# Performance work log

Measured on AMD Instinct MI355X. Metric: run time of the kernel, lower is better.

Reference implementation:

```python
import jax, jax.numpy as jnp
import numpy as np

N, IN_F, OUT_F, G = 8192, 1024, 1024, 5


def setup_inputs() -> dict:
    key = jax.random.key(0)
    k1, k2 = jax.random.split(key)
    x = jax.random.normal(k1, (N, IN_F), dtype=jnp.float32)
    spline_weights = jax.random.normal(k2, (OUT_F, IN_F, G), dtype=jnp.float32) * 0.1
    return {"x": x, "spline_weights": spline_weights}


def reference(x, spline_weights):
    out_f, in_f, g = spline_weights.shape
    grid = jnp.linspace(-1.0, 1.0, g).astype(x.dtype)
    leading = x.shape[:-1]
    xf = x.reshape(-1, in_f)                       # [N, in]
    x_c = jnp.clip(jnp.tanh(xf), grid[0], grid[-1])
    # bucket index: number of grid points <= x_c, minus 1, clamped to [0, g-2]
    idx = jnp.sum(x_c[..., None] >= grid, axis=-1) - 1
    idx = jnp.clip(idx, 0, g - 2)                  # [N, in] int
    idx_r = jnp.minimum(idx + 1, g - 1)
    g_left = grid[idx]
    g_right = grid[idx_r]
    t = (x_c - g_left) / (g_right - g_left + 1e-8)  # [N, in]
    # sparse interpolation coefficients over the grid axis: two nonzeros per (n,i)
    oh_l = jax.nn.one_hot(idx, g, dtype=xf.dtype)   # [N, in, G]
    oh_r = jax.nn.one_hot(idx_r, g, dtype=xf.dtype)
    coeff = (1.0 - t)[..., None] * oh_l + t[..., None] * oh_r  # [N, in, G]
    # y[n,o] = sum_i (1-t) * W[o,i,idx] + t * W[o,i,idx+1]
    out = jnp.einsum('nig,oig->no', coeff, spline_weights)
    return out.reshape(*leading, out_f)
```

## Files before the change

### kernel.cpp

```cpp
#include <hip/hip_runtime.h>
#include <stdint.h>

#define N_ROWS 8192
#define IN_F   1024
#define OUT_F  1024
#define NG     5
#define KTOT   (IN_F * NG)

#define BM 128
#define BN 128
#define BK 64
#define NKT (KTOT / BK)

typedef float          f32x4 __attribute__((ext_vector_type(4)));
typedef short          s16x8 __attribute__((ext_vector_type(8)));
typedef unsigned short u16x8 __attribute__((ext_vector_type(8)));

__device__ __forceinline__ unsigned short f2bf_rne(float f) {
    unsigned u = __float_as_uint(f);
    u = (u + 0x7fffu + ((u >> 16) & 1u)) >> 16;
    return (unsigned short)u;
}
__device__ __forceinline__ float bf2f(unsigned short h) {
    return __uint_as_float(((unsigned)h) << 16);
}

__device__ __forceinline__ void gload_lds16(const void* g, void* l) {
    __builtin_amdgcn_global_load_lds(
        (const __attribute__((address_space(1))) unsigned int*)g,
        (__attribute__((address_space(3))) unsigned int*)l, 16, 0, 0);
}

__global__ __launch_bounds__(256) void prep_p(const float* __restrict__ x,
                                              unsigned short* __restrict__ P) {
    int t = blockIdx.x * 256 + threadIdx.x;
    float4 v = reinterpret_cast<const float4*>(x)[t];
    float r[4] = {v.x, v.y, v.z, v.w};
    ushort4 o;
    unsigned short* po = (unsigned short*)&o;
#pragma unroll
    for (int j = 0; j < 4; ++j) {
        float xc = fminf(fmaxf(r[j], -9.0f), 9.0f);
        float e  = __expf(2.0f * xc);
        float th = (e - 1.0f) / (e + 1.0f);
        po[j] = (unsigned short)__float2uint_rn((th + 1.0f) * 32767.0f);
    }
    reinterpret_cast<ushort4*>(P)[t] = o;
}

__global__ __launch_bounds__(256) void prep_w(const float* __restrict__ W,
                                              unsigned short* __restrict__ Wh,
                                              unsigned short* __restrict__ Wl) {
    int t = blockIdx.x * 256 + threadIdx.x;
    int o = t >> 10, i = t & 1023;
    const float* wp = W + (size_t)o * KTOT + i * NG;
#pragma unroll
    for (int g = 0; g < NG; ++g) {
        float w = wp[g];
        unsigned short h = f2bf_rne(w);
        unsigned short l = f2bf_rne(w - bf2f(h));
        int dst = o * KTOT + g * 1024 + i;
        Wh[dst] = h;
        Wl[dst] = l;
    }
}

struct SLds {
    unsigned short Ah[BM * BK];
    unsigned short Al[BM * BK];
    unsigned short Bh[BN * BK];
    unsigned short Bl[BN * BK];
};

__global__ __launch_bounds__(256, 2) void kan_gemm(
        const unsigned short* __restrict__ P,
        const unsigned short* __restrict__ Wh,
        const unsigned short* __restrict__ Wl,
        float* __restrict__ out) {
    __shared__ SLds s;

    int bid = blockIdx.x;
    int wg  = (bid & 7) * 64 + (bid >> 3);
    int nb  = wg >> 6;
    int mb  = wg & 63;
    int n0 = mb * BM, o0 = nb * BN;

    int tid  = threadIdx.x;
    int lane = tid & 63, wid = tid >> 6;
    int wm = wid >> 1, wn = wid & 1;

    int aoff[4], adst[4];
#pragma unroll
    for (int r = 0; r < 4; ++r) {
        int f = tid + r * 256, row = f >> 3, ks = f & 7;
        aoff[r] = (n0 + row) * IN_F + ks * 8;
        adst[r] = row * BK + ((ks ^ (row & 7)) << 3);
    }
    int bks = (lane & 7) ^ (lane >> 3);
    int boff[4];
#pragma unroll
    for (int q = 0; q < 4; ++q)
        boff[q] = (o0 + wid * 32 + q * 8 + (lane >> 3)) * KTOT + bks * 8;
    int arow_f = wm * 64 + (lane & 15);
    int brow_f = wn * 64 + (lane & 15);
    int sl0    = lane >> 4;

    f32x4 acc[4][4] = {};

    u16x8 ucur[4], unext[4];
#pragma unroll
    for (int r = 0; r < 4; ++r)
        ucur[r] = *reinterpret_cast<const u16x8*>(&P[aoff[r]]);

    for (int kt = 0; kt < NKT; ++kt) {
        int k0 = kt * BK;
        int g  = k0 >> 10;
        float gv = -1.0f + 0.5f * (float)g;
        int i0n = ((kt + 1 < NKT) ? (kt + 1) * BK : 0) & 1023;

        __syncthreads();

#pragma unroll
        for (int q = 0; q < 4; ++q) {
            int ldsrow = (wid * 32 + q * 8) * BK;
            gload_lds16(Wh + boff[q] + k0, &s.Bh[ldsrow]);
            gload_lds16(Wl + boff[q] + k0, &s.Bl[ldsrow]);
        }
#pragma unroll
        for (int r = 0; r < 4; ++r)
            unext[r] = *reinterpret_cast<const u16x8*>(&P[aoff[r] + i0n]);

#pragma unroll
        for (int r = 0; r < 4; ++r) {
            u16x8 hv, lv;
#pragma unroll
            for (int j = 0; j < 8; ++j) {
                float xc = fmaf((float)ucur[r][j], (1.0f / 32767.0f), -1.0f);
                float c  = fmaxf(0.0f, fmaf(-2.0f, fabsf(xc - gv), 1.0f));
                unsigned hb = __float_as_uint(c) >> 16;
                hv[j] = (unsigned short)hb;
                float hi = __uint_as_float(hb << 16);
                lv[j] = (unsigned short)(__float_as_uint(c - hi) >> 16);
            }
            *reinterpret_cast<u16x8*>(&s.Ah[adst[r]]) = hv;
            *reinterpret_cast<u16x8*>(&s.Al[adst[r]]) = lv;
        }
#pragma unroll
        for (int r = 0; r < 4; ++r) ucur[r] = unext[r];

        __syncthreads();

#pragma unroll
        for (int kk = 0; kk < 2; ++kk) {
            s16x8 ah[4], al[4], bh[4], bl[4];
#pragma unroll
            for (int m = 0; m < 4; ++m) {
                int row  = arow_f + m * 16;
                int slot = (kk * 4 + sl0) ^ (row & 7);
                ah[m] = *reinterpret_cast<const s16x8*>(&s.Ah[row * BK + slot * 8]);
                al[m] = *reinterpret_cast<const s16x8*>(&s.Al[row * BK + slot * 8]);
            }
#pragma unroll
            for (int nf = 0; nf < 4; ++nf) {
                int row  = brow_f + nf * 16;
                int slot = (kk * 4 + sl0) ^ (row & 7);
                bh[nf] = *reinterpret_cast<const s16x8*>(&s.Bh[row * BK + slot * 8]);
                bl[nf] = *reinterpret_cast<const s16x8*>(&s.Bl[row * BK + slot * 8]);
            }
#pragma unroll
            for (int m = 0; m < 4; ++m)
#pragma unroll
                for (int nf = 0; nf < 4; ++nf) {
                    acc[m][nf] = __builtin_amdgcn_mfma_f32_16x16x32_bf16(
                                     ah[m], bh[nf], acc[m][nf], 0, 0, 0);
                    acc[m][nf] = __builtin_amdgcn_mfma_f32_16x16x32_bf16(
                                     ah[m], bl[nf], acc[m][nf], 0, 0, 0);
                    acc[m][nf] = __builtin_amdgcn_mfma_f32_16x16x32_bf16(
                                     al[m], bh[nf], acc[m][nf], 0, 0, 0);
                }
        }
    }

    int rb = n0 + wm * 64 + (lane >> 4) * 4;
    int cb = o0 + wn * 64 + (lane & 15);
#pragma unroll
    for (int m = 0; m < 4; ++m)
#pragma unroll
        for (int nf = 0; nf < 4; ++nf)
#pragma unroll
            for (int jj = 0; jj < 4; ++jj)
                out[(size_t)(rb + m * 16 + jj) * OUT_F + cb + nf * 16] =
                    acc[m][nf][jj];
}

__global__ __launch_bounds__(256) void kan_naive(const float* __restrict__ x,
                                                 const float* __restrict__ W,
                                                 float* __restrict__ out) {
    int bn = blockIdx.x & 3;
    int bm = blockIdx.x >> 2;
    int o = bn * 256 + threadIdx.x;
    int nbase = bm * 16;
    float acc[16];
#pragma unroll
    for (int j = 0; j < 16; ++j) acc[j] = 0.0f;
    for (int i = 0; i < IN_F; ++i) {
        const float* wp = &W[(size_t)o * KTOT + i * NG];
        float w0 = wp[0], w1 = wp[1], w2 = wp[2], w3 = wp[3], w4 = wp[4];
#pragma unroll
        for (int j = 0; j < 16; ++j) {
            float xc = tanhf(x[(size_t)(nbase + j) * IN_F + i]);
            float c0 = fmaxf(0.f, fmaf(-2.f, fabsf(xc + 1.0f), 1.f));
            float c1 = fmaxf(0.f, fmaf(-2.f, fabsf(xc + 0.5f), 1.f));
            float c2 = fmaxf(0.f, fmaf(-2.f, fabsf(xc), 1.f));
            float c3 = fmaxf(0.f, fmaf(-2.f, fabsf(xc - 0.5f), 1.f));
            float c4 = fmaxf(0.f, fmaf(-2.f, fabsf(xc - 1.0f), 1.f));
            acc[j] += c0 * w0 + c1 * w1 + c2 * w2 + c3 * w3 + c4 * w4;
        }
    }
#pragma unroll
    for (int j = 0; j < 16; ++j)
        out[(size_t)(nbase + j) * OUT_F + o] = acc[j];
}

extern "C" void kernel_launch(void* const* d_in, const int* in_sizes, int n_in,
                              void* d_out, int out_size, void* d_ws, size_t ws_size,
                              hipStream_t stream) {
    const float* x = (const float*)d_in[0];
    const float* W = (const float*)d_in[1];
    float* out = (float*)d_out;

    const size_t P_BYTES = (size_t)N_ROWS * IN_F * 2;
    const size_t WPLANE  = (size_t)OUT_F * KTOT * 2;

    if (ws_size >= P_BYTES + 2 * WPLANE) {
        unsigned short* P  = (unsigned short*)d_ws;
        unsigned short* Wh = (unsigned short*)((char*)d_ws + P_BYTES);
        unsigned short* Wl = (unsigned short*)((char*)d_ws + P_BYTES + WPLANE);
        prep_p<<<(N_ROWS * IN_F / 4) / 256, 256, 0, stream>>>(x, P);
        prep_w<<<(OUT_F * IN_F) / 256, 256, 0, stream>>>(W, Wh, Wl);
        kan_gemm<<<512, 256, 0, stream>>>(P, Wh, Wl, out);
    } else {
        kan_naive<<<2048, 256, 0, stream>>>(x, W, out);
    }
}
```

Measured before the change: 307.7 us.

## Precompute A hi/lo planes and double-buffer a pure async-LDS GEMM

When the workspace is large enough, a new prep kernel expands tanh(x) into full bf16 hi/lo coefficient planes over all grid points. A pure GEMM then streams both A and B into LDS with direct global-to-LDS loads, double-buffered with BK=32 and one barrier per step. This removes per-tile coefficient computation and the register staging of A from the main loop. The cost is a larger workspace and more HBM traffic, since the A planes are about 5x wider than the quantized P. A mid fallback kernel with a different tile shape and a vectorized prep_w are also added.

```diff
diff --git a/kernel.cpp b/kernel.cpp
--- a/kernel.cpp
+++ b/kernel.cpp
@@ -7,11 +7,6 @@
 #define NG     5
 #define KTOT   (IN_F * NG)
 
-#define BM 128
-#define BN 128
-#define BK 64
-#define NKT (KTOT / BK)
-
 typedef float          f32x4 __attribute__((ext_vector_type(4)));
 typedef short          s16x8 __attribute__((ext_vector_type(8)));
 typedef unsigned short u16x8 __attribute__((ext_vector_type(8)));
@@ -24,60 +19,88 @@
 __device__ __forceinline__ float bf2f(unsigned short h) {
     return __uint_as_float(((unsigned)h) << 16);
 }
-
 __device__ __forceinline__ void gload_lds16(const void* g, void* l) {
     __builtin_amdgcn_global_load_lds(
         (const __attribute__((address_space(1))) unsigned int*)g,
         (__attribute__((address_space(3))) unsigned int*)l, 16, 0, 0);
 }
 
-__global__ __launch_bounds__(256) void prep_p(const float* __restrict__ x,
-                                              unsigned short* __restrict__ P) {
+__global__ __launch_bounds__(256) void prep_a(const float* __restrict__ x,
+                                              unsigned short* __restrict__ Ahp,
+                                              unsigned short* __restrict__ Alp) {
     int t = blockIdx.x * 256 + threadIdx.x;
-    float4 v = reinterpret_cast<const float4*>(x)[t];
-    float r[4] = {v.x, v.y, v.z, v.w};
-    ushort4 o;
-    unsigned short* po = (unsigned short*)&o;
-#pragma unroll
-    for (int j = 0; j < 4; ++j) {
-        float xc = fminf(fmaxf(r[j], -9.0f), 9.0f);
-        float e  = __expf(2.0f * xc);
-        float th = (e - 1.0f) / (e + 1.0f);
-        po[j] = (unsigned short)__float2uint_rn((th + 1.0f) * 32767.0f);
-    }
-    reinterpret_cast<ushort4*>(P)[t] = o;
+    int n = t >> 7, i8 = t & 127;
+    const float4* xp = reinterpret_cast<const float4*>(x + (size_t)n * IN_F + i8 * 8);
+    float4 a = xp[0], b = xp[1];
+    float r[8] = {a.x, a.y, a.z, a.w, b.x, b.y, b.z, b.w};
+    float xc[8];
+#pragma unroll
+    for (int j = 0; j < 8; ++j) {
+        float v = fminf(fmaxf(r[j], -9.0f), 9.0f);
+        float e = __expf(2.0f * v);
+        xc[j] = (e - 1.0f) / (e + 1.0f);
+    }
+    size_t base = (size_t)n * KTOT + i8 * 8;
+#pragma unroll
+    for (int g = 0; g < NG; ++g) {
+        float gv = -1.0f + 0.5f * (float)g;
+        u16x8 hv, lv;
+#pragma unroll
+        for (int j = 0; j < 8; ++j) {
+            float c  = fmaxf(0.0f, fmaf(-2.0f, fabsf(xc[j] - gv), 1.0f));
+            unsigned hb = __float_as_uint(c) >> 16;
+            hv[j] = (unsigned short)hb;
+            lv[j] = (unsigned short)(__float_as_uint(c - __uint_as_float(hb << 16)) >> 16);
+        }
+        *reinterpret_cast<u16x8*>(&Ahp[base + g * 1024]) = hv;
+        *reinterpret_cast<u16x8*>(&Alp[base + g * 1024]) = lv;
+    }
 }
 
 __global__ __launch_bounds__(256) void prep_w(const float* __restrict__ W,
                                               unsigned short* __restrict__ Wh,
                                               unsigned short* __restrict__ Wl) {
-    int t = blockIdx.x * 256 + threadIdx.x;
-    int o = t >> 10, i = t & 1023;
-    const float* wp = W + (size_t)o * KTOT + i * NG;
+    int t  = blockIdx.x * 256 + threadIdx.x;
+    int o  = t >> 8, i4 = (t & 255) * 4;
+    const float4* wp = reinterpret_cast<const float4*>(W + (size_t)o * KTOT + i4 * NG);
+    float f[20];
+#pragma unroll
+    for (int q = 0; q < 5; ++q) {
+        float4 v = wp[q];
+        f[q*4+0] = v.x; f[q*4+1] = v.y; f[q*4+2] = v.z; f[q*4+3] = v.w;
+    }
 #pragma unroll
     for (int g = 0; g < NG; ++g) {
-        float w = wp[g];
-        unsigned short h = f2bf_rne(w);
-        unsigned short l = f2bf_rne(w - bf2f(h));
-        int dst = o * KTOT + g * 1024 + i;
-        Wh[dst] = h;
-        Wl[dst] = l;
-    }
-}
-
-struct SLds {
-    unsigned short Ah[BM * BK];
-    unsigned short Al[BM * BK];
-    unsigned short Bh[BN * BK];
-    unsigned short Bl[BN * BK];
-};
-
-__global__ __launch_bounds__(256, 2) void kan_gemm(
-        const unsigned short* __restrict__ P,
+        ushort4 hq, lq;
+        unsigned short* hp = (unsigned short*)&hq;
+        unsigned short* lp = (unsigned short*)&lq;
+#pragma unroll
+        for (int di = 0; di < 4; ++di) {
+            float w = f[di * NG + g];
+            unsigned short h = f2bf_rne(w);
+            hp[di] = h;
+            lp[di] = f2bf_rne(w - bf2f(h));
+        }
+        int dst = o * KTOT + g * 1024 + i4;
+        *reinterpret_cast<ushort4*>(&Wh[dst]) = hq;
+        *reinterpret_cast<ushort4*>(&Wl[dst]) = lq;
+    }
+}
+
+#define BM 128
+#define BN 128
+#define PBK 32
+#define PNKT (KTOT / PBK)
+
+struct SLdsDB { unsigned short d[2][4][BM * PBK]; };
+
+__global__ __launch_bounds__(256, 2) void kan_gemm_pure(
+        const unsigned short* __restrict__ Ahp,
+        const unsigned short* __restrict__ Alp,
         const unsigned short* __restrict__ Wh,
         const unsigned short* __restrict__ Wl,
         float* __restrict__ out) {
-    __shared__ SLds s;
+    __shared__ SLdsDB s;
 
     int bid = blockIdx.x;
     int wg  = (bid & 7) * 64 + (bid >> 3);
@@ -89,100 +112,192 @@
     int lane = tid & 63, wid = tid >> 6;
     int wm = wid >> 1, wn = wid & 1;
 
-    int aoff[4], adst[4];
-#pragma unroll
-    for (int r = 0; r < 4; ++r) {
-        int f = tid + r * 256, row = f >> 3, ks = f & 7;
-        aoff[r] = (n0 + row) * IN_F + ks * 8;
-        adst[r] = row * BK + ((ks ^ (row & 7)) << 3);
-    }
-    int bks = (lane & 7) ^ (lane >> 3);
-    int boff[4];
+    int ks = (lane & 3) ^ ((lane >> 3) & 3);
+    int gA[2], gB[2], ldsb[2];
+#pragma unroll
+    for (int q = 0; q < 2; ++q) {
+        int r = wid * 32 + q * 16 + (lane >> 2);
+        gA[q] = (n0 + r) * KTOT + ks * 8;
+        gB[q] = (o0 + r) * KTOT + ks * 8;
+        ldsb[q] = (wid * 32 + q * 16) * PBK;
+    }
+    int sl0  = lane >> 4;
+    int arow = wm * 64 + (lane & 15);
+    int brow = wn * 64 + (lane & 15);
+    int aaddr = arow * PBK + ((sl0 ^ ((arow >> 1) & 3)) << 3);
+    int baddr = brow * PBK + ((sl0 ^ ((brow >> 1) & 3)) << 3);
+
+    f32x4 acc[4][4] = {};
+
+    auto STAGE = [&](int buf, int k0) {
+#pragma unroll
+        for (int q = 0; q < 2; ++q) {
+            gload_lds16(Ahp + gA[q] + k0, &s.d[buf][0][ldsb[q]]);
+            gload_lds16(Alp + gA[q] + k0, &s.d[buf][1][ldsb[q]]);
+            gload_lds16(Wh  + gB[q] + k0, &s.d[buf][2][ldsb[q]]);
+            gload_lds16(Wl  + gB[q] + k0, &s.d[buf][3][ldsb[q]]);
+        }
+    };
+    auto COMPUTE = [&](int buf) {
+        s16x8 ah[4], al[4], bh[4], bl[4];
+#pragma unroll
+        for (int m = 0; m < 4; ++m) {
+            ah[m] = *reinterpret_cast<const s16x8*>(&s.d[buf][0][aaddr + m * 512]);
+            al[m] = *reinterpret_cast<const s16x8*>(&s.d[buf][1][aaddr + m * 512]);
+        }
+#pragma unroll
+        for (int nf = 0; nf < 4; ++nf) {
+            bh[nf] = *reinterpret_cast<const s16x8*>(&s.d[buf][2][baddr + nf * 512]);
+            bl[nf] = *reinterpret_cast<const s16x8*>(&s.d[buf][3][baddr + nf * 512]);
+        }
+#pragma unroll
+        for (int m = 0; m < 4; ++m)
+#pragma unroll
+            for (int nf = 0; nf < 4; ++nf) {
+                acc[m][nf] = __builtin_amdgcn_mfma_f32_16x16x32_bf16(
+                                 ah[m], bh[nf], acc[m][nf], 0, 0, 0);
+                acc[m][nf] = __builtin_amdgcn_mfma_f32_16x16x32_bf16(
+                                 ah[m], bl[nf], acc[m][nf], 0, 0, 0);
+                acc[m][nf] = __builtin_amdgcn_mfma_f32_16x16x32_bf16(
+                                 al[m], bh[nf], acc[m][nf], 0, 0, 0);
+            }
+    };
+
+    STAGE(0, 0);
+    __syncthreads();
+    int cur = 0;
+    for (int kt = 0; kt < PNKT - 1; ++kt) {
+        STAGE(cur ^ 1, (kt + 1) * PBK);
+        COMPUTE(cur);
+        __syncthreads();
+        cur ^= 1;
+    }
+    COMPUTE(cur);
+
+    int rb = n0 + wm * 64 + (lane >> 4) * 4;
+    int cb = o0 + wn * 64 + (lane & 15);
+#pragma unroll
+    for (int m = 0; m < 4; ++m)
+#pragma unroll
+        for (int nf = 0; nf < 4; ++nf)
+#pragma unroll
+            for (int jj = 0; jj < 4; ++jj)
+                out[(size_t)(rb + m * 16 + jj) * OUT_F + cb + nf * 16] =
+                    acc[m][nf][jj];
+}
+
+__global__ __launch_bounds__(256) void prep_p(const float* __restrict__ x,
+                                              unsigned short* __restrict__ P) {
+    int t = blockIdx.x * 256 + threadIdx.x;
+    float4 a = reinterpret_cast<const float4*>(x)[t * 2];
+    float4 b = reinterpret_cast<const float4*>(x)[t * 2 + 1];
+    float r[8] = {a.x, a.y, a.z, a.w, b.x, b.y, b.z, b.w};
+    u16x8 o;
+#pragma unroll
+    for (int j = 0; j < 8; ++j) {
+        float xc = fminf(fmaxf(r[j], -9.0f), 9.0f);
+        float e  = __expf(2.0f * xc);
+        float th = (e - 1.0f) / (e + 1.0f);
+        o[j] = (unsigned short)__float2uint_rn((th + 1.0f) * 32767.0f);
+    }
+    *reinterpret_cast<u16x8*>(&P[(size_t)t * 8]) = o;
+}
+
+#define MBM 64
+#define MBN 256
+#define MBK 32
+struct SLdsM {
+    unsigned short Ah[4 * MBM * 8];
+    unsigned short Al[4 * MBM * 8];
+    unsigned short Bh[4 * MBN * 8];
+    unsigned short Bl[4 * MBN * 8];
+};
+
+__global__ __launch_bounds__(256, 3) void kan_gemm_mid(
+        const unsigned short* __restrict__ P,
+        const unsigned short* __restrict__ Wh,
+        const unsigned short* __restrict__ Wl,
+        float* __restrict__ out) {
+    __shared__ SLdsM s;
+    int bid = blockIdx.x;
+    int wg  = (bid & 7) * 64 + (bid >> 3);
+    int nb  = wg >> 7, mb = wg & 127;
+    int n0 = mb * MBM, o0 = nb * MBN;
+    int tid  = threadIdx.x;
+    int lane = tid & 63, w = tid >> 6;
+
+    int arow = tid >> 2, aks = tid & 3;
+    int agoff = (n0 + arow) * IN_F + aks * 8;
+    int aldst = aks * (MBM * 8) + arow * 8;
+    int brow4 = tid >> 2, bchunk = tid & 3;
+    int bldst = bchunk * (MBN * 8) + brow4 * 8;
+    int bgq[4];
 #pragma unroll
     for (int q = 0; q < 4; ++q)
-        boff[q] = (o0 + wid * 32 + q * 8 + (lane >> 3)) * KTOT + bks * 8;
-    int arow_f = wm * 64 + (lane & 15);
-    int brow_f = wn * 64 + (lane & 15);
-    int sl0    = lane >> 4;
+        bgq[q] = (o0 + q * 64 + brow4) * KTOT + bchunk * 8;
+    int fchunk = lane >> 4, fr = lane & 15;
 
     f32x4 acc[4][4] = {};
-
-    u16x8 ucur[4], unext[4];
-#pragma unroll
-    for (int r = 0; r < 4; ++r)
-        ucur[r] = *reinterpret_cast<const u16x8*>(&P[aoff[r]]);
-
-    for (int kt = 0; kt < NKT; ++kt) {
-        int k0 = kt * BK;
-        int g  = k0 >> 10;
-        float gv = -1.0f + 0.5f * (float)g;
-        int i0n = ((kt + 1 < NKT) ? (kt + 1) * BK : 0) & 1023;
-
+    for (int kt = 0; kt < KTOT / MBK; ++kt) {
+        int k0 = kt * MBK;
+        float gv = -1.0f + 0.5f * (float)(kt >> 5);
+        int i0 = (kt & 31) * MBK;
         __syncthreads();
-
-#pragma unroll
-        for (int q = 0; q < 4; ++q) {
-            int ldsrow = (wid * 32 + q * 8) * BK;
-            gload_lds16(Wh + boff[q] + k0, &s.Bh[ldsrow]);
-            gload_lds16(Wl + boff[q] + k0, &s.Bl[ldsrow]);
-        }
-#pragma unroll
-        for (int r = 0; r < 4; ++r)
-            unext[r] = *reinterpret_cast<const u16x8*>(&P[aoff[r] + i0n]);
-
-#pragma unroll
-        for (int r = 0; r < 4; ++r) {
+        u16x8 bregh[4], bregl[4];
+#pragma unroll
+        for (int q = 0; q < 4; ++q)
+            bregh[q] = *reinterpret_cast<const u16x8*>(&Wh[bgq[q] + k0]);
+#pragma unroll
+        for (int q = 0; q < 4; ++q)
+            bregl[q] = *reinterpret_cast<const u16x8*>(&Wl[bgq[q] + k0]);
+        {
+            u16x8 u = *reinterpret_cast<const u16x8*>(&P[agoff + i0]);
             u16x8 hv, lv;
 #pragma unroll
             for (int j = 0; j < 8; ++j) {
-                float xc = fmaf((float)ucur[r][j], (1.0f / 32767.0f), -1.0f);
+                float xc = fmaf((float)u[j], (1.0f / 32767.0f), -1.0f);
                 float c  = fmaxf(0.0f, fmaf(-2.0f, fabsf(xc - gv), 1.0f));
                 unsigned hb = __float_as_uint(c) >> 16;
                 hv[j] = (unsigned short)hb;
-                float hi = __uint_as_float(hb << 16);
-                lv[j] = (unsigned short)(__float_as_uint(c - hi) >> 16);
+                lv[j] = (unsigned short)(__float_as_uint(c - __uint_as_float(hb << 16)) >> 16);
             }
-            *reinterpret_cast<u16x8*>(&s.Ah[adst[r]]) = hv;
-            *reinterpret_cast<u16x8*>(&s.Al[adst[r]]) = lv;
-        }
-#pragma unroll
-        for (int r = 0; r < 4; ++r) ucur[r] = unext[r];
-
+            *reinterpret_cast<u16x8*>(&s.Ah[aldst]) = hv;
+            *reinterpret_cast<u16x8*>(&s.Al[aldst]) = lv;
+        }
+#pragma unroll
+        for (int q = 0; q < 4; ++q) {
+            *reinterpret_cast<u16x8*>(&s.Bh[bldst + q * 512]) = bregh[q];
+            *reinterpret_cast<u16x8*>(&s.Bl[bldst + q * 512]) = bregl[q];
+        }
         __syncthreads();
 
-#pragma unroll
-        for (int kk = 0; kk < 2; ++kk) {
-            s16x8 ah[4], al[4], bh[4], bl[4];
-#pragma unroll
-            for (int m = 0; m < 4; ++m) {
-                int row  = arow_f + m * 16;
-                int slot = (kk * 4 + sl0) ^ (row & 7);
-                ah[m] = *reinterpret_cast<const s16x8*>(&s.Ah[row * BK + slot * 8]);
-                al[m] = *reinterpret_cast<const s16x8*>(&s.Al[row * BK + slot * 8]);
+        s16x8 ah[4], al[4], bh[4], bl[4];
+#pragma unroll
+        for (int m = 0; m < 4; ++m) {
+            int e = fchunk * (MBM * 8) + (m * 16 + fr) * 8;
+            ah[m] = *reinterpret_cast<const s16x8*>(&s.Ah[e]);
+            al[m] = *reinterpret_cast<const s16x8*>(&s.Al[e]);
+        }
+#pragma unroll
+        for (int nf = 0; nf < 4; ++nf) {
+            int e = fchunk * (MBN * 8) + (w * 64 + nf * 16 + fr) * 8;
+            bh[nf] = *reinterpret_cast<const s16x8*>(&s.Bh[e]);
+            bl[nf] = *reinterpret_cast<const s16x8*>(&s.Bl[e]);
+        }
+#pragma unroll
+        for (int m = 0; m < 4; ++m)
+#pragma unroll
+            for (int nf = 0; nf < 4; ++nf) {
+                acc[m][nf] = __builtin_amdgcn_mfma_f32_16x16x32_bf16(
+                                 ah[m], bh[nf], acc[m][nf], 0, 0, 0);
+                acc[m][nf] = __builtin_amdgcn_mfma_f32_16x16x32_bf16(
+                                 ah[m], bl[nf], acc[m][nf], 0, 0, 0);
+                acc[m][nf] = __builtin_amdgcn_mfma_f32_16x16x32_bf16(
+                                 al[m], bh[nf], acc[m][nf], 0, 0, 0);
             }
-#pragma unroll
-            for (int nf = 0; nf < 4; ++nf) {
-                int row  = brow_f + nf * 16;
-                int slot = (kk * 4 + sl0) ^ (row & 7);
-                bh[nf] = *reinterpret_cast<const s16x8*>(&s.Bh[row * BK + slot * 8]);
-                bl[nf] = *reinterpret_cast<const s16x8*>(&s.Bl[row * BK + slot * 8]);
-            }
-#pragma unroll
-            for (int m = 0; m < 4; ++m)
-#pragma unroll
-                for (int nf = 0; nf < 4; ++nf) {
-                    acc[m][nf] = __builtin_amdgcn_mfma_f32_16x16x32_bf16(
-                                     ah[m], bh[nf], acc[m][nf], 0, 0, 0);
-                    acc[m][nf] = __builtin_amdgcn_mfma_f32_16x16x32_bf16(
-                                     ah[m], bl[nf], acc[m][nf], 0, 0, 0);
-                    acc[m][nf] = __builtin_amdgcn_mfma_f32_16x16x32_bf16(
-                                     al[m], bh[nf], acc[m][nf], 0, 0, 0);
-                }
-        }
-    }
-
-    int rb = n0 + wm * 64 + (lane >> 4) * 4;
-    int cb = o0 + wn * 64 + (lane & 15);
+    }
+    int rb = n0 + (lane >> 4) * 4;
+    int cb = o0 + w * 64 + (lane & 15);
 #pragma unroll
     for (int m = 0; m < 4; ++m)
 #pragma unroll
@@ -229,16 +344,25 @@
     const float* W = (const float*)d_in[1];
     float* out = (float*)d_out;
 
+    const size_t APLANE  = (size_t)N_ROWS * KTOT * 2;
+    const size_t WPLANE  = (size_t)OUT_F * KTOT * 2;
     const size_t P_BYTES = (size_t)N_ROWS * IN_F * 2;
-    const size_t WPLANE  = (size_t)OUT_F * KTOT * 2;
-
-    if (ws_size >= P_BYTES + 2 * WPLANE) {
+
+    if (ws_size >= 2 * APLANE + 2 * WPLANE) {
+        unsigned short* Ahp = (unsigned short*)d_ws;
+        unsigned short* Alp = (unsigned short*)((char*)d_ws + APLANE);
+        unsigned short* Wh  = (unsigned short*)((char*)d_ws + 2 * APLANE);
+        unsigned short* Wl  = (unsigned short*)((char*)d_ws + 2 * APLANE + WPLANE);
+        prep_a<<<(N_ROWS * IN_F / 8) / 256, 256, 0, stream>>>(x, Ahp, Alp);
+        prep_w<<<(OUT_F * IN_F / 4) / 256, 256, 0, stream>>>(W, Wh, Wl);
+        kan_gemm_pure<<<512, 256, 0, stream>>>(Ahp, Alp, Wh, Wl, out);
+    } else if (ws_size >= P_BYTES + 2 * WPLANE) {
         unsigned short* P  = (unsigned short*)d_ws;
         unsigned short* Wh = (unsigned short*)((char*)d_ws + P_BYTES);
         unsigned short* Wl = (unsigned short*)((char*)d_ws + P_BYTES + WPLANE);
-        prep_p<<<(N_ROWS * IN_F / 4) / 256, 256, 0, stream>>>(x, P);
-        prep_w<<<(OUT_F * IN_F) / 256, 256, 0, stream>>>(W, Wh, Wl);
-        kan_gemm<<<512, 256, 0, stream>>>(P, Wh, Wl, out);
+        prep_p<<<(N_ROWS * IN_F / 8) / 256, 256, 0, stream>>>(x, P);
+        prep_w<<<(OUT_F * IN_F / 4) / 256, 256, 0, stream>>>(W, Wh, Wl);
+        kan_gemm_mid<<<512, 256, 0, stream>>>(P, Wh, Wl, out);
     } else {
         kan_naive<<<2048, 256, 0, stream>>>(x, W, out);
     }
```

After: 374.9 us. 21.9% more time.
